# Kernel tuning notes

Measured on AMD Instinct MI355X. Metric: run time of the kernel, lower is better.

## Reference

```python
import jax, jax.numpy as jnp
import numpy as np

DEPTH, DIM, DH, H, DQ, V = 4, 1024, 4096, 8, 128, 32000
B, L = 2, 1024


def setup_inputs() -> dict:
    key = jax.random.key(0)
    ks = iter(jax.random.split(key, 48))
    def nrm(shape, scale=1.0):
        return jax.random.normal(next(ks), shape, jnp.float32) * scale
    d = {}
    d["x"] = nrm((B, L, V))
    d["tin_w"] = nrm((DIM, V), V ** -0.5)
    d["tin_b"] = nrm((DIM,), 0.02)
    d["tout_w"] = nrm((V, DIM), DIM ** -0.5)
    d["tout_b"] = nrm((V,), 0.02)
    d["wq_w"] = nrm((DEPTH, H * DQ, DIM), DIM ** -0.5)
    d["wq_b"] = nrm((DEPTH, H * DQ), 0.02)
    d["wk_w"] = nrm((DEPTH, H * DQ, DIM), DIM ** -0.5)
    d["wk_b"] = nrm((DEPTH, H * DQ), 0.02)
    d["wv_w"] = nrm((DEPTH, H * DQ, DIM), DIM ** -0.5)
    d["wv_b"] = nrm((DEPTH, H * DQ), 0.02)
    d["wo_w"] = nrm((DEPTH, DIM, H * DQ), (H * DQ) ** -0.5)
    d["wo_b"] = nrm((DEPTH, DIM), 0.02)
    d["f1_w"] = nrm((DEPTH, DH, DIM), DIM ** -0.5)
    d["f1_b"] = nrm((DEPTH, DH), 0.02)
    d["f2_w"] = nrm((DEPTH, DIM, DH), DH ** -0.5)
    d["f2_b"] = nrm((DEPTH, DIM), 0.02)
    d["phz_re"] = nrm((DEPTH, H, DQ))
    d["phz_im"] = nrm((DEPTH, H, DQ))
    d["amp"] = nrm((DEPTH, H))
    d["lc_re"] = nrm((DEPTH, H, DQ, DQ), 0.02)
    d["lc_im"] = nrm((DEPTH, H, DQ, DQ), 0.02)
    return d


def _layernorm(x):
    m = x.mean(-1, keepdims=True)
    v = ((x - m) ** 2).mean(-1, keepdims=True)
    return (x - m) * jax.lax.rsqrt(v + 1e-5)


def _retention(x, qw, qb, kw, kb, vw, vb, ow, ob, pre, pim, amp, lcr, lci):
    b, l, _ = x.shape
    q = (x @ qw.T + qb).reshape(b, l, H, DQ)
    k = (x @ kw.T + kb).reshape(b, l, H, DQ)
    v = (x @ vw.T + vb).reshape(b, l, H, DQ)
    pz = pre + 1j * pim                              # [H,DQ] complex
    phase = pz / jnp.abs(pz)                         # unit modulus
    a = jax.nn.sigmoid(amp)                          # [H]
    phazor = phase * a[:, None]
    n = jnp.arange(l)
    pp = phase[None, :, :] ** n[:, None, None]       # [L,H,DQ]
    pp_inv = phase[None, :, :] ** (-n)[:, None, None]
    php = phazor[None, :, :] ** n[:, None, None]
    lc = jax.lax.stop_gradient(lcr + 1j * lci)       # [H,DQ,DQ], detached in torch
    qc = q.astype(jnp.complex64)
    kc = k.astype(jnp.complex64)
    vc = v.astype(jnp.complex64)
    cross = jnp.einsum('blhd,lhd,hde->blhe', qc, php * phazor[None], lc)
    tril = n[:, None] >= n[None, :]
    expn = jnp.where(tril, n[:, None] - n[None, :], 0)           # [L,L]
    mask = jnp.where(tril[None], a[:, None, None] ** expn[None], 0.0)  # [H,L,L]
    qk = jnp.einsum('blhd,bmhd->bhlm', qc * pp[None], kc * pp_inv[None])
    inner = jnp.einsum('bhlm,bmhd->blhd', qk * mask[None].astype(jnp.complex64), vc)
    y = jax.nn.silu((inner + cross).real).reshape(b, l, H * DQ)
    return y @ ow.T + ob


def reference(x, tin_w, tin_b, tout_w, tout_b, wq_w, wq_b, wk_w, wk_b, wv_w, wv_b,
              wo_w, wo_b, f1_w, f1_b, f2_w, f2_b, phz_re, phz_im, amp, lc_re, lc_im):
    h = x @ tin_w.T + tin_b
    for i in range(DEPTH):
        r = _retention(_layernorm(h), wq_w[i], wq_b[i], wk_w[i], wk_b[i],
                       wv_w[i], wv_b[i], wo_w[i], wo_b[i],
                       phz_re[i], phz_im[i], amp[i], lc_re[i], lc_im[i])
        h = h + r
        f = _layernorm(h)
        f = jax.nn.silu(f @ f1_w[i].T + f1_b[i]) @ f2_w[i].T + f2_b[i]
        h = h + f
    return h @ tout_w.T + tout_b
```

## Files before the change

### kernel.cpp

```cpp
#include <hip/hip_runtime.h>
#include <hip/hip_bf16.h>
#include <stdint.h>

#define DEPTH 4
#define DIM   1024
#define DH    4096
#define NH    8
#define DQ    128
#define VOC   32000
#define BATCH 2
#define SEQ   1024
#define ROWS  (BATCH*SEQ)

#define PQKV  ((long long)ROWS*DIM)
#define PQKV3 ((long long)ROWS*3*DIM)
#define PROT  ((long long)BATCH*NH*SEQ*2*DQ)
#define PVT   ((long long)BATCH*NH*DQ*SEQ)
#define PS    ((long long)BATCH*NH*SEQ*SEQ)
#define PMID  ((long long)ROWS*DH)
#define PY    ((long long)ROWS*DIM)

typedef __hip_bfloat16 bf16;
using f32x4  = __attribute__((ext_vector_type(4))) float;
using bf16x8 = __attribute__((ext_vector_type(8))) __bf16;

__device__ __forceinline__ void wpair(bf16* p, long long off, long long plane, float v) {
  bf16 hi = __float2bfloat16(v);
  p[off] = hi;
  p[off + plane] = __float2bfloat16(v - __bfloat162float(hi));
}

__device__ __forceinline__ void gload_lds16(const void* g, void* l) {
  __builtin_amdgcn_global_load_lds(
      (const __attribute__((address_space(1))) void*)g,
      (__attribute__((address_space(3))) void*)(uintptr_t)l,
      16, 0, 0);
}

#define BM 128
#define BN 128
#define BKK 64
#define PL 16384

template<int EPI, int SA, int SB>
__global__ __launch_bounds__(256, (SA || SB) ? 2 : 4)
void gemm_bt(const bf16* __restrict__ A, long long sA, long long pA, int lda,
             const bf16* __restrict__ B, long long sB, long long pB, int ldb, int bmod,
             void* __restrict__ Cv, long long sC, long long pC, int ldc,
             const float* __restrict__ bias, int hmod,
             int M, int N, int K, int ksplit, int causal)
{
  __shared__ int4 sbuf[1024 * (2 + SA + SB)];
  char* Asb = (char*)sbuf;
  char* Bsb = Asb + PL * (1 + SA);

  const int tid  = threadIdx.x;
  const int lane = tid & 63;
  const int wave = tid >> 6;
  const int wr   = wave >> 1;
  const int wc   = wave & 1;
  const int z    = blockIdx.z;
  const int zb   = z / ksplit;
  const int ks   = z - zb * ksplit;
  const int Kc   = K / ksplit;
  const int k0   = ks * Kc;
  const int tm   = blockIdx.x * BM;
  const int tn   = blockIdx.y * BN;

  if (causal == 1 && tn >= tm + BM) return;
  int kend = k0 + Kc;
  if (causal == 2) {
    kend = min(kend, tm + BM);
    if (kend <= k0) return;
  }

  const bf16* Ab = A + (long long)zb * sA;
  const bf16* Bb = B + (long long)(zb % bmod) * sB;

  f32x4 acc[4][4] = {};

  for (int kt = k0; kt < kend; kt += BKK) {
#pragma unroll
    for (int j = 0; j < 4; ++j) {
      int slot0 = j*256 + wave*64;
      int i = slot0 + lane;
      int row = i >> 3;
      int gc  = (i & 7) ^ (row & 7);
      long long ga = (long long)(tm + row) * lda + kt + gc*8;
      long long gb = (long long)(tn + row) * ldb + kt + gc*8;
      gload_lds16(Ab + ga, Asb + slot0*16);
      if (SA) gload_lds16(Ab + pA + ga, Asb + PL + slot0*16);
      gload_lds16(Bb + gb, Bsb + slot0*16);
      if (SB) gload_lds16(Bb + pB + gb, Bsb + PL + slot0*16);
    }
    __syncthreads();
#pragma unroll
    for (int kh = 0; kh < 2; ++kh) {
      const int cb = kh*4 + (lane >> 4);
      int4 avh[4], bvh[4], avl[4], bvl[4];
#pragma unroll
      for (int mi = 0; mi < 4; ++mi) {
        int m = wr*64 + mi*16 + (lane & 15);
        int off = m*128 + ((cb ^ (m & 7)) << 4);
        avh[mi] = *(const int4*)(Asb + off);
        if (SA) avl[mi] = *(const int4*)(Asb + PL + off);
      }
#pragma unroll
      for (int nj = 0; nj < 4; ++nj) {
        int n = wc*64 + nj*16 + (lane & 15);
        int off = n*128 + ((cb ^ (n & 7)) << 4);
        bvh[nj] = *(const int4*)(Bsb + off);
        if (SB) bvl[nj] = *(const int4*)(Bsb + PL + off);
      }
#pragma unroll
      for (int mi = 0; mi < 4; ++mi)
#pragma unroll
        for (int nj = 0; nj < 4; ++nj)
          acc[mi][nj] = __builtin_amdgcn_mfma_f32_16x16x32_bf16(
              __builtin_bit_cast(bf16x8, avh[mi]),
              __builtin_bit_cast(bf16x8, bvh[nj]), acc[mi][nj], 0, 0, 0);
      if (SA)
#pragma unroll
        for (int mi = 0; mi < 4; ++mi)
#pragma unroll
          for (int nj = 0; nj < 4; ++nj)
            acc[mi][nj] = __builtin_amdgcn_mfma_f32_16x16x32_bf16(
                __builtin_bit_cast(bf16x8, avl[mi]),
                __builtin_bit_cast(bf16x8, bvh[nj]), acc[mi][nj], 0, 0, 0);
      if (SB)
#pragma unroll
        for (int mi = 0; mi < 4; ++mi)
#pragma unroll
          for (int nj = 0; nj < 4; ++nj)
            acc[mi][nj] = __builtin_amdgcn_mfma_f32_16x16x32_bf16(
                __builtin_bit_cast(bf16x8, avh[mi]),
                __builtin_bit_cast(bf16x8, bvl[nj]), acc[mi][nj], 0, 0, 0);
    }
    __syncthreads();
  }

  const float* dtab = (EPI == 7) ? bias + (zb % hmod) * (SEQ + 1) : nullptr;
  const int col = lane & 15;
  const int rb  = (lane >> 4) << 2;
  float* Cf = (float*)Cv + (long long)zb * sC;
  bf16*  Ch = (bf16*) Cv + (long long)zb * sC;

#pragma unroll
  for (int mi = 0; mi < 4; ++mi)
#pragma unroll
    for (int nj = 0; nj < 4; ++nj) {
      long long gn = tn + wc*64 + nj*16 + col;
      float bv_ = (EPI != 7 && bias && ks == 0) ? bias[gn] : 0.f;
#pragma unroll
      for (int r = 0; r < 4; ++r) {
        long long gm = tm + wr*64 + mi*16 + rb + r;
        float v = acc[mi][nj][r] + bv_;
        long long off = gm * (long long)ldc + gn;
        if (EPI == 0)      Cf[off] = v;
        else if (EPI == 3) { if (ksplit > 1) atomicAdd(&Cf[off], v); else Cf[off] += v; }
        else if (EPI == 5) wpair(Ch, off, pC, v);
        else if (EPI == 6) wpair(Ch, off, pC, v / (1.f + __expf(-v)));
        else {
          long long dlt = gm - gn;
          float dcy = (dlt >= 0) ? dtab[dlt] : 0.f;
          Ch[off] = __float2bfloat16(acc[mi][nj][r] * dcy);
        }
      }
    }
}

__global__ void castw_kernel(const float* __restrict__ wq, const float* __restrict__ wk,
                             const float* __restrict__ wv, const float* __restrict__ wo,
                             const float* __restrict__ f1, const float* __restrict__ f2,
                             bf16* __restrict__ Wqkv, bf16* __restrict__ Wol,
                             bf16* __restrict__ Wf1, bf16* __restrict__ Wf2) {
  const long long S1 = (long long)DIM*DIM;
  const long long WP = 3*S1;
  long long i = (long long)blockIdx.x * blockDim.x + threadIdx.x;
  if (i < 3*S1) {
    const float* src = (i < S1) ? wq : (i < 2*S1) ? wk : wv;
    float v = src[i & (S1-1)];
    bf16 h = __float2bfloat16(v);
    Wqkv[i] = h;
    Wqkv[i + WP] = __float2bfloat16(v - __bfloat162float(h));
  } else if (i < 4*S1) {
    long long j = i - 3*S1;
    float v = wo[j];
    bf16 h = __float2bfloat16(v);
    Wol[j] = h;
    Wol[j + S1] = __float2bfloat16(v - __bfloat162float(h));
  } else if (i < 8*S1) {
    long long j = i - 4*S1;
    float v = f1[j];
    bf16 h = __float2bfloat16(v);
    Wf1[j] = h;
    Wf1[j + 4*S1] = __float2bfloat16(v - __bfloat162float(h));
  } else if (i < 12*S1) {
    long long j = i - 8*S1;
    Wf2[j] = __float2bfloat16(f2[j]);
  }
}

#define MISC_LC   (NH*DQ*DQ)
#define MISC_B3   (MISC_LC + 3*DIM)
#define MISC_DC   (MISC_B3 + NH*(SEQ+1))
#define MISC_ZR   (MISC_DC + (BATCH*NH*SEQ*DQ)/4)
__global__ void misc_kernel(const float* __restrict__ lcr, const float* __restrict__ lci,
                            bf16* __restrict__ lc,
                            const float* __restrict__ bq, const float* __restrict__ bk,
                            const float* __restrict__ bv, float* __restrict__ qkvbi,
                            const float* __restrict__ amp, float* __restrict__ dtab,
                            float4* __restrict__ retz) {
  long long i = (long long)blockIdx.x * blockDim.x + threadIdx.x;
  if (i < MISC_LC) {
    int d = i & 127, e = (i >> 7) & 127, h = i >> 14;
    float vr = lcr[((long long)h*DQ + d)*DQ + e];
    float vi = lci[((long long)h*DQ + d)*DQ + e];
    long long dst = ((long long)h*DQ + e)*(2*DQ) + d;
    lc[dst]      = __float2bfloat16(vr);
    lc[dst + DQ] = __float2bfloat16(-vi);
  } else if (i < MISC_B3) {
    int j = (int)(i - MISC_LC);
    qkvbi[j] = (j < DIM) ? bq[j] : (j < 2*DIM) ? bk[j - DIM] : bv[j - 2*DIM];
  } else if (i < MISC_DC) {
    int j = (int)(i - MISC_B3);
    int h = j / (SEQ+1), n = j % (SEQ+1);
    float a = 1.f / (1.f + __expf(-amp[h]));
    dtab[j] = powf(a, (float)n);
  } else if (i < MISC_ZR) {
    retz[i - MISC_DC] = float4{0.f, 0.f, 0.f, 0.f};
  }
}

#define TIN_X4 ((long long)ROWS*VOC/4)
#define TIN_W4 (TIN_X4 + (long long)DIM*VOC/4)
#define TIN_H4 (TIN_W4 + (long long)ROWS*DIM/4)
__global__ void tinprep_kernel(const float* __restrict__ x, bf16* __restrict__ xb,
                               const float* __restrict__ tw, bf16* __restrict__ twb,
                               float4* __restrict__ hz) {
  long long i = (long long)blockIdx.x * blockDim.x + threadIdx.x;
  const float* src; bf16* dst; long long j;
  if (i < TIN_X4)      { src = x;  dst = xb;  j = i; }
  else if (i < TIN_W4) { src = tw; dst = twb; j = i - TIN_X4; }
  else if (i < TIN_H4) { hz[i - TIN_W4] = float4{0.f,0.f,0.f,0.f}; return; }
  else return;
  float4 v = ((const float4*)src)[j];
  ushort4 o{__builtin_bit_cast(unsigned short, __float2bfloat16(v.x)),
            __builtin_bit_cast(unsigned short, __float2bfloat16(v.y)),
            __builtin_bit_cast(unsigned short, __float2bfloat16(v.z)),
            __builtin_bit_cast(unsigned short, __float2bfloat16(v.w))};
  ((ushort4*)dst)[j] = o;
}

#define TAIL_H (PQKV)
#define TAIL_W (TAIL_H + (long long)VOC*DIM/4)
__global__ void tailprep_kernel(const float* __restrict__ h, bf16* __restrict__ hb,
                                const float* __restrict__ tw, bf16* __restrict__ twb) {
  long long i = (long long)blockIdx.x * blockDim.x + threadIdx.x;
  if (i < TAIL_H) {
    float v = h[i];
    bf16 hi = __float2bfloat16(v);
    hb[i] = hi;
    hb[i + PQKV] = __float2bfloat16(v - __bfloat162float(hi));
  } else if (i < TAIL_W) {
    long long j = i - TAIL_H;
    float4 v = ((const float4*)tw)[j];
    ushort4 o{__builtin_bit_cast(unsigned short, __float2bfloat16(v.x)),
              __builtin_bit_cast(unsigned short, __float2bfloat16(v.y)),
              __builtin_bit_cast(unsigned short, __float2bfloat16(v.z)),
              __builtin_bit_cast(unsigned short, __float2bfloat16(v.w))};
    ((ushort4*)twb)[j] = o;
  }
}

__global__ void ln_kernel(const float* __restrict__ in, bf16* __restrict__ out) {
  const int row = blockIdx.x;
  const int tid = threadIdx.x;
  const float4 v = ((const float4*)(in + (size_t)row*DIM))[tid];
  float s  = v.x + v.y + v.z + v.w;
  float s2 = v.x*v.x + v.y*v.y + v.z*v.z + v.w*v.w;
#pragma unroll
  for (int o = 32; o > 0; o >>= 1) { s += __shfl_xor(s, o); s2 += __shfl_xor(s2, o); }
  __shared__ float red[8];
  const int wv = tid >> 6;
  if ((tid & 63) == 0) { red[wv] = s; red[4 + wv] = s2; }
  __syncthreads();
  s  = red[0] + red[1] + red[2] + red[3];
  s2 = red[4] + red[5] + red[6] + red[7];
  const float mean = s * (1.f / DIM);
  const float var  = s2 * (1.f / DIM) - mean * mean;
  const float inv  = rsqrtf(var + 1e-5f);
  long long base = (long long)row*DIM + tid*4;
  wpair(out, base + 0, PQKV, (v.x - mean) * inv);
  wpair(out, base + 1, PQKV, (v.y - mean) * inv);
  wpair(out, base + 2, PQKV, (v.z - mean) * inv);
  wpair(out, base + 3, PQKV, (v.w - mean) * inv);
}

__global__ void rotate_kernel(const bf16* __restrict__ qkv,
                              const float* __restrict__ pre, const float* __restrict__ pim,
                              const float* __restrict__ dtab,
                              bf16* __restrict__ qrot, bf16* __restrict__ krot,
                              bf16* __restrict__ qwb) {
  const int d = threadIdx.x, l = blockIdx.x, h = blockIdx.y, b = blockIdx.z;
  const float tr = pre[h*DQ + d], ti = pim[h*DQ + d];
  const float theta = atan2f(ti, tr);
  const long long rowb = (long long)(b*SEQ + l)*(3*DIM) + h*DQ + d;
  const float qv = __bfloat162float(qkv[rowb]) + __bfloat162float(qkv[rowb + PQKV3]);
  const float kv = __bfloat162float(qkv[rowb + DIM]) + __bfloat162float(qkv[rowb + DIM + PQKV3]);
  float sn, cs;
  sincosf(theta * (float)l, &sn, &cs);
  const long long dst = ((long long)(b*NH + h)*SEQ + l)*(2*DQ) + d;
  qrot[dst]      = __float2bfloat16(qv * cs);
  qrot[dst + DQ] = __float2bfloat16(qv * sn);
  krot[dst]      = __float2bfloat16(kv * cs);
  krot[dst + DQ] = __float2bfloat16(kv * sn);
  float sn2, cs2;
  sincosf(theta * (float)(l + 1), &sn2, &cs2);
  const float ad = dtab[h*(SEQ+1) + l + 1];
  qwb[dst]      = __float2bfloat16(qv * ad * cs2);
  qwb[dst + DQ] = __float2bfloat16(qv * ad * sn2);
}

__global__ void vt_kernel(const bf16* __restrict__ qkv, bf16* __restrict__ vt) {
  __shared__ float tile[64][65];
  const int t  = threadIdx.x;
  const int c  = t & 63, r4 = t >> 6;
  const int m0 = blockIdx.x * 64;
  const int d0 = blockIdx.y * 64;
  const int h  = blockIdx.z & (NH - 1);
  const int b  = blockIdx.z >> 3;
#pragma unroll
  for (int rr = 0; rr < 64; rr += 4) {
    const int m = m0 + rr + r4;
    const long long src = (long long)(b*SEQ + m)*(3*DIM) + 2*DIM + h*DQ + d0 + c;
    tile[rr + r4][c] = __bfloat162float(qkv[src]) + __bfloat162float(qkv[src + PQKV3]);
  }
  __syncthreads();
#pragma unroll
  for (int rr = 0; rr < 64; rr += 4) {
    const int d = rr + r4;
    vt[((long long)(b*NH + h)*DQ + d0 + d)*SEQ + m0 + c] = __float2bfloat16(tile[c][d]);
  }
}

__global__ void siluret_kernel(const float* __restrict__ ret, bf16* __restrict__ y) {
  const int d = threadIdx.x, l = blockIdx.x, h = blockIdx.y, b = blockIdx.z;
  float r = ret[((long long)(b*NH + h)*SEQ + l)*DQ + d];
  float s = r / (1.f + __expf(-r));
  wpair(y, ((long long)(b*SEQ + l)*NH + h)*DQ + d, PY, s);
}

extern "C" void kernel_launch(void* const* d_in, const int* in_sizes, int n_in,
                              void* d_out, int out_size, void* d_ws, size_t ws_size,
                              hipStream_t stream) {
  const float* x      = (const float*)d_in[0];
  const float* tin_w  = (const float*)d_in[1];
  const float* tin_b  = (const float*)d_in[2];
  const float* tout_w = (const float*)d_in[3];
  const float* tout_b = (const float*)d_in[4];
  const float* wq_w   = (const float*)d_in[5];
  const float* wq_b   = (const float*)d_in[6];
  const float* wk_w   = (const float*)d_in[7];
  const float* wk_b   = (const float*)d_in[8];
  const float* wv_w   = (const float*)d_in[9];
  const float* wv_b   = (const float*)d_in[10];
  const float* wo_w   = (const float*)d_in[11];
  const float* wo_b   = (const float*)d_in[12];
  const float* f1_w   = (const float*)d_in[13];
  const float* f1_b   = (const float*)d_in[14];
  const float* f2_w   = (const float*)d_in[15];
  const float* f2_b   = (const float*)d_in[16];
  const float* phz_re = (const float*)d_in[17];
  const float* phz_im = (const float*)d_in[18];
  const float* amp    = (const float*)d_in[19];
  const float* lc_re  = (const float*)d_in[20];
  const float* lc_im  = (const float*)d_in[21];
  (void)in_sizes; (void)n_in; (void)out_size; (void)ws_size;

  char* w = (char*)d_ws;
  auto alloc = [&](size_t bytes) {
    char* p = w; w += (bytes + 255) & ~(size_t)255; return p;
  };
  auto palloc = [&](long long elems) {
    return (bf16*)alloc((size_t)elems * 2 * 2);
  };

  const long long WP = 3LL*DIM*DIM;
  float* h     = (float*)alloc((size_t)ROWS*DIM*4);
  float* ret   = (float*)alloc((size_t)BATCH*NH*SEQ*DQ*4);
  float* qkvbi = (float*)alloc((size_t)3*DIM*4);
  float* dtab  = (float*)alloc((size_t)NH*(SEQ+1)*4);
  bf16*  hb    = palloc(PQKV);
  bf16*  Wqkv  = palloc(WP);
  bf16*  Wol   = palloc((long long)DIM*DIM);
  bf16*  Wf1l  = palloc((long long)DH*DIM);
  bf16*  Wf2l  = (bf16*)alloc((size_t)DIM*DH*2);
  bf16*  qkvb  = palloc(PQKV3);
  bf16*  lcc   = (bf16*)alloc((size_t)NH*DQ*2*DQ*2);
  bf16*  Wbig  = (bf16*)alloc((size_t)DIM*VOC*2);
  bf16*  qrot  = (bf16*)alloc((size_t)PROT*2);
  bf16*  krot  = (bf16*)alloc((size_t)PROT*2);
  bf16*  qwb   = (bf16*)alloc((size_t)PROT*2);
  bf16*  vtb   = (bf16*)alloc((size_t)PVT*2);
  bf16*  Sb    = (bf16*)alloc((size_t)PS*2);
  bf16*  mid   = palloc(PMID);
  bf16*  xb = (bf16*)d_out;
  bf16*  yb = qkvb;

  auto gemm = [&](int epi, int sa, int sb, const bf16* A, long long sA, long long pA, int lda,
                  const bf16* B, long long sB, long long pB, int ldb, int bmod,
                  void* C, long long sC, long long pC, int ldc,
                  const float* bias, int hmod, int M, int N, int K, int batch,
                  int ksplit, int causal) {
    dim3 g(M / BM, N / BN, batch * ksplit), blk(256);
    if (epi == 3 && !sa && !sb)      gemm_bt<3,0,0><<<g, blk, 0, stream>>>(A,sA,pA,lda,B,sB,pB,ldb,bmod,C,sC,pC,ldc,bias,hmod,M,N,K,ksplit,causal);
    else if (epi == 7)               gemm_bt<7,0,0><<<g, blk, 0, stream>>>(A,sA,pA,lda,B,sB,pB,ldb,bmod,C,sC,pC,ldc,bias,hmod,M,N,K,ksplit,causal);
    else if (epi == 0 && sa && !sb)  gemm_bt<0,1,0><<<g, blk, 0, stream>>>(A,sA,pA,lda,B,sB,pB,ldb,bmod,C,sC,pC,ldc,bias,hmod,M,N,K,ksplit,causal);
    else if (epi == 3 && sa && !sb)  gemm_bt<3,1,0><<<g, blk, 0, stream>>>(A,sA,pA,lda,B,sB,pB,ldb,bmod,C,sC,pC,ldc,bias,hmod,M,N,K,ksplit,causal);
    else if (epi == 3)               gemm_bt<3,1,1><<<g, blk, 0, stream>>>(A,sA,pA,lda,B,sB,pB,ldb,bmod,C,sC,pC,ldc,bias,hmod,M,N,K,ksplit,causal);
    else if (epi == 5)               gemm_bt<5,1,1><<<g, blk, 0, stream>>>(A,sA,pA,lda,B,sB,pB,ldb,bmod,C,sC,pC,ldc,bias,hmod,M,N,K,ksplit,causal);
    else if (epi == 6)               gemm_bt<6,1,1><<<g, blk, 0, stream>>>(A,sA,pA,lda,B,sB,pB,ldb,bmod,C,sC,pC,ldc,bias,hmod,M,N,K,ksplit,causal);
  };
  const int BIG = 1 << 30;

  {
    long long tot = TIN_H4;
    tinprep_kernel<<<dim3((unsigned)((tot + 255) / 256)), dim3(256), 0, stream>>>(
        x, xb, tin_w, Wbig, (float4*)h);
  }
  gemm(3, 0, 0, xb, 0, 0, VOC, Wbig, 0, 0, VOC, BIG, h, 0, 0, DIM, tin_b, 1,
       ROWS, DIM, VOC, 1, 10, 0);

  for (int i = 0; i < DEPTH; ++i) {
    {
      long long tot = 12LL*DIM*DIM;
      castw_kernel<<<dim3((unsigned)((tot + 255) / 256)), dim3(256), 0, stream>>>(
          wq_w + (size_t)i*DIM*DIM, wk_w + (size_t)i*DIM*DIM, wv_w + (size_t)i*DIM*DIM,
          wo_w + (size_t)i*DIM*DIM, f1_w + (size_t)i*DH*DIM, f2_w + (size_t)i*DIM*DH,
          Wqkv, Wol, Wf1l, Wf2l);
      misc_kernel<<<dim3((unsigned)((MISC_ZR + 255) / 256)), dim3(256), 0, stream>>>(
          lc_re + (size_t)i*NH*DQ*DQ, lc_im + (size_t)i*NH*DQ*DQ, lcc,
          wq_b + i*DIM, wk_b + i*DIM, wv_b + i*DIM, qkvbi,
          amp + i*NH, dtab, (float4*)ret);
    }

    ln_kernel<<<ROWS, 256, 0, stream>>>(h, hb);
    gemm(5, 1, 1, hb, 0, PQKV, DIM, Wqkv, 0, WP, DIM, BIG,
         qkvb, 0, PQKV3, 3*DIM, qkvbi, 1, ROWS, 3*DIM, DIM, 1, 1, 0);
    rotate_kernel<<<dim3(SEQ, NH, BATCH), DQ, 0, stream>>>(
        qkvb, phz_re + i*NH*DQ, phz_im + i*NH*DQ, dtab, qrot, krot, qwb);
    vt_kernel<<<dim3(SEQ/64, DQ/64, BATCH*NH), 256, 0, stream>>>(qkvb, vtb);
    gemm(7, 0, 0, qrot, (long long)SEQ*2*DQ, 0, 2*DQ,
         krot, (long long)SEQ*2*DQ, 0, 2*DQ, BIG,
         Sb, (long long)SEQ*SEQ, 0, SEQ, dtab, NH, SEQ, SEQ, 2*DQ, BATCH*NH, 1, 1);
    gemm(3, 0, 0, Sb, (long long)SEQ*SEQ, 0, SEQ,
         vtb, (long long)DQ*SEQ, 0, SEQ, BIG,
         ret, (long long)SEQ*DQ, 0, DQ, nullptr, 1, SEQ, DQ, SEQ, BATCH*NH, 4, 2);
    gemm(3, 0, 0, qwb, (long long)SEQ*2*DQ, 0, 2*DQ,
         lcc, (long long)DQ*2*DQ, 0, 2*DQ, NH,
         ret, (long long)SEQ*DQ, 0, DQ, nullptr, 1, SEQ, DQ, 2*DQ, BATCH*NH, 2, 0);
    siluret_kernel<<<dim3(SEQ, NH, BATCH), DQ, 0, stream>>>(ret, yb);
    gemm(3, 1, 1, yb, 0, PY, DIM, Wol, 0, (long long)DIM*DIM, DIM, BIG,
         h, 0, 0, DIM, wo_b + i*DIM, 1, ROWS, DIM, DIM, 1, 2, 0);

    ln_kernel<<<ROWS, 256, 0, stream>>>(h, hb);
    gemm(6, 1, 1, hb, 0, PQKV, DIM, Wf1l, 0, (long long)DH*DIM, DIM, BIG,
         mid, 0, PMID, DH, f1_b + i*DH, 1, ROWS, DH, DIM, 1, 1, 0);
    gemm(3, 1, 0, mid, 0, PMID, DH, Wf2l, 0, 0, DH, BIG,
         h, 0, 0, DIM, f2_b + i*DIM, 1, ROWS, DIM, DH, 1, 4, 0);
  }

  tailprep_kernel<<<dim3((unsigned)((TAIL_W + 255) / 256)), dim3(256), 0, stream>>>(
      h, hb, tout_w, Wbig);
  gemm(0, 1, 0, hb, 0, PQKV, DIM, Wbig, 0, 0, DIM, BIG,
       (float*)d_out, 0, 0, VOC, tout_b, 1, ROWS, VOC, DIM, 1, 1, 0);
}
```

Before: 1.864 ms.

## Add 256x256-tile double-buffered MFMA GEMM for token-in, FFN2 and output projections

Adds a new 512-thread GEMM kernel with 256x256 output tiles, XOR-swizzled LDS staged through direct global-to-LDS loads, double buffering, and explicit waitcnt/barrier scheduling with raised priority around MFMA blocks. It replaces the 128x128 gemm_bt for the large-K input projection, the FFN down projection (now split 8 ways with atomics), and the vocabulary output projection. The split-precision A operand (hi/lo planes) is handled by running K as multiple passes over offset planes. The larger tiles are meant to raise arithmetic intensity and cut global traffic, at the cost of more LDS per block and fewer blocks in flight.

```diff
diff --git a/kernel.cpp b/kernel.cpp
--- a/kernel.cpp
+++ b/kernel.cpp
@@ -35,6 +35,134 @@
       (const __attribute__((address_space(1))) void*)g,
       (__attribute__((address_space(3))) void*)(uintptr_t)l,
       16, 0, 0);
+}
+
+#define VMW(n) asm volatile("s_waitcnt vmcnt(" #n ")" ::: "memory")
+
+template<int EPI, int NPASS>
+__global__ __launch_bounds__(512, 2)
+void gemm256(const bf16* __restrict__ A, long long aoff1, long long aoff2, int lda,
+             const bf16* __restrict__ B, long long boff1, long long boff2, int ldb,
+             float* __restrict__ C, int ldc,
+             const float* __restrict__ bias,
+             int M, int N, int K, int ksplit)
+{
+  __shared__ char sh[131072];
+  const int tid  = threadIdx.x;
+  const int lane = tid & 63;
+  const int wid  = tid >> 6;
+  const int wr   = wid >> 2;
+  const int wc   = wid & 3;
+  const int z    = blockIdx.z;
+  const int tm   = blockIdx.x * 256;
+  const int tn   = blockIdx.y * 256;
+  const int nt   = (K * NPASS / 64) / ksplit;
+  const int g0   = z * nt;
+
+  auto stage = [&](int g, int b, int u) {
+    int kt = g * 64;
+    long long ao = 0, bo = 0;
+    if (NPASS >= 2 && kt >= K) {
+      if (NPASS >= 3 && kt >= 2*K) { ao = aoff2; bo = boff2; kt -= 2*K; }
+      else                         { ao = aoff1; bo = boff1; kt -= K; }
+    }
+    int mat, s;
+    switch (u) { case 0: mat=0; s=0; break;  case 1: mat=0; s=2; break;
+                 case 2: mat=1; s=0; break;  case 3: mat=1; s=1; break;
+                 case 4: mat=1; s=2; break;  case 5: mat=1; s=3; break;
+                 case 6: mat=0; s=1; break;  default: mat=0; s=3; break; }
+    int row = s*64 + (tid >> 3);
+    int gc  = (tid & 7) ^ (row & 7);
+    const bf16* src = mat
+        ? (B + bo + (long long)(tn + row) * ldb + kt + gc*8)
+        : (A + ao + (long long)(tm + row) * lda + kt + gc*8);
+    gload_lds16(src, sh + b*65536 + mat*32768 + s*8192 + wid*1024);
+  };
+  auto rdA = [&](int b, int mf, int ks) -> int4 {
+    int m = wr*128 + mf*16 + (lane & 15);
+    int c = ks*4 + (lane >> 4);
+    return *(const int4*)(sh + b*65536 + m*128 + ((c ^ (m & 7)) << 4));
+  };
+  auto rdB = [&](int b, int g, int ks) -> int4 {
+    int n = wc*64 + g*16 + (lane & 15);
+    int c = ks*4 + (lane >> 4);
+    return *(const int4*)(sh + b*65536 + 32768 + n*128 + ((c ^ (n & 7)) << 4));
+  };
+
+  f32x4 acc[8][4] = {};
+  int4  bfr[2][4];
+
+#pragma unroll
+  for (int u = 0; u < 8; ++u) stage(g0, 0, u);
+  VMW(2);
+  __builtin_amdgcn_s_barrier();
+  __builtin_amdgcn_sched_barrier(0);
+
+  for (int j = 0; j < nt; ++j) {
+    const int  b    = j & 1;
+    const bool more = (j + 1 < nt);
+    const int  gn1  = g0 + j + 1;
+#pragma unroll
+    for (int q = 0; q < 4; ++q) {
+      const int mf0 = 2*q, mf1 = 2*q + 1;
+      int4 a00 = rdA(b, mf0, 0), a01 = rdA(b, mf0, 1);
+      int4 a10 = rdA(b, mf1, 0), a11 = rdA(b, mf1, 1);
+      if (q == 0) {
+#pragma unroll
+        for (int ks = 0; ks < 2; ++ks)
+#pragma unroll
+          for (int g = 0; g < 4; ++g) bfr[ks][g] = rdB(b, g, ks);
+      }
+      if (more) { stage(gn1, b^1, 2*q); stage(gn1, b^1, 2*q + 1); }
+      __builtin_amdgcn_s_barrier();
+      asm volatile("s_waitcnt lgkmcnt(0)" ::: "memory");
+      __builtin_amdgcn_sched_barrier(0);
+      __builtin_amdgcn_s_setprio(1);
+#pragma unroll
+      for (int g = 0; g < 4; ++g)
+        acc[mf0][g] = __builtin_amdgcn_mfma_f32_16x16x32_bf16(
+            __builtin_bit_cast(bf16x8, a00), __builtin_bit_cast(bf16x8, bfr[0][g]),
+            acc[mf0][g], 0, 0, 0);
+#pragma unroll
+      for (int g = 0; g < 4; ++g)
+        acc[mf0][g] = __builtin_amdgcn_mfma_f32_16x16x32_bf16(
+            __builtin_bit_cast(bf16x8, a01), __builtin_bit_cast(bf16x8, bfr[1][g]),
+            acc[mf0][g], 0, 0, 0);
+#pragma unroll
+      for (int g = 0; g < 4; ++g)
+        acc[mf1][g] = __builtin_amdgcn_mfma_f32_16x16x32_bf16(
+            __builtin_bit_cast(bf16x8, a10), __builtin_bit_cast(bf16x8, bfr[0][g]),
+            acc[mf1][g], 0, 0, 0);
+#pragma unroll
+      for (int g = 0; g < 4; ++g)
+        acc[mf1][g] = __builtin_amdgcn_mfma_f32_16x16x32_bf16(
+            __builtin_bit_cast(bf16x8, a11), __builtin_bit_cast(bf16x8, bfr[1][g]),
+            acc[mf1][g], 0, 0, 0);
+      __builtin_amdgcn_s_setprio(0);
+      if (q == 1) { if (more) VMW(4); else VMW(0); }
+      if (q == 3) { if (more) VMW(2); }
+      __builtin_amdgcn_s_barrier();
+      __builtin_amdgcn_sched_barrier(0);
+    }
+  }
+
+  const int col = lane & 15;
+  const int rb  = (lane >> 4) << 2;
+#pragma unroll
+  for (int mf = 0; mf < 8; ++mf)
+#pragma unroll
+    for (int g = 0; g < 4; ++g) {
+      long long gn = tn + wc*64 + g*16 + col;
+      float bv = (z == 0 && bias) ? bias[gn] : 0.f;
+#pragma unroll
+      for (int r = 0; r < 4; ++r) {
+        long long gm = tm + wr*128 + mf*16 + rb + r;
+        long long off = gm * (long long)ldc + gn;
+        float v = acc[mf][g][r] + bv;
+        if (EPI == 0) C[off] = v;
+        else { if (ksplit > 1) atomicAdd(&C[off], v); else C[off] += v; }
+      }
+    }
 }
 
 #define BM 128
@@ -416,7 +544,6 @@
     dim3 g(M / BM, N / BN, batch * ksplit), blk(256);
     if (epi == 3 && !sa && !sb)      gemm_bt<3,0,0><<<g, blk, 0, stream>>>(A,sA,pA,lda,B,sB,pB,ldb,bmod,C,sC,pC,ldc,bias,hmod,M,N,K,ksplit,causal);
     else if (epi == 7)               gemm_bt<7,0,0><<<g, blk, 0, stream>>>(A,sA,pA,lda,B,sB,pB,ldb,bmod,C,sC,pC,ldc,bias,hmod,M,N,K,ksplit,causal);
-    else if (epi == 0 && sa && !sb)  gemm_bt<0,1,0><<<g, blk, 0, stream>>>(A,sA,pA,lda,B,sB,pB,ldb,bmod,C,sC,pC,ldc,bias,hmod,M,N,K,ksplit,causal);
     else if (epi == 3 && sa && !sb)  gemm_bt<3,1,0><<<g, blk, 0, stream>>>(A,sA,pA,lda,B,sB,pB,ldb,bmod,C,sC,pC,ldc,bias,hmod,M,N,K,ksplit,causal);
     else if (epi == 3)               gemm_bt<3,1,1><<<g, blk, 0, stream>>>(A,sA,pA,lda,B,sB,pB,ldb,bmod,C,sC,pC,ldc,bias,hmod,M,N,K,ksplit,causal);
     else if (epi == 5)               gemm_bt<5,1,1><<<g, blk, 0, stream>>>(A,sA,pA,lda,B,sB,pB,ldb,bmod,C,sC,pC,ldc,bias,hmod,M,N,K,ksplit,causal);
@@ -424,26 +551,20 @@
   };
   const int BIG = 1 << 30;
 
-  {
-    long long tot = TIN_H4;
-    tinprep_kernel<<<dim3((unsigned)((tot + 255) / 256)), dim3(256), 0, stream>>>(
-        x, xb, tin_w, Wbig, (float4*)h);
-  }
-  gemm(3, 0, 0, xb, 0, 0, VOC, Wbig, 0, 0, VOC, BIG, h, 0, 0, DIM, tin_b, 1,
-       ROWS, DIM, VOC, 1, 10, 0);
+  tinprep_kernel<<<dim3((unsigned)((TIN_H4 + 255) / 256)), dim3(256), 0, stream>>>(
+      x, xb, tin_w, Wbig, (float4*)h);
+  gemm256<3,1><<<dim3(ROWS/256, DIM/256, 10), dim3(512), 0, stream>>>(
+      xb, 0, 0, VOC, Wbig, 0, 0, VOC, h, DIM, tin_b, ROWS, DIM, VOC, 10);
 
   for (int i = 0; i < DEPTH; ++i) {
-    {
-      long long tot = 12LL*DIM*DIM;
-      castw_kernel<<<dim3((unsigned)((tot + 255) / 256)), dim3(256), 0, stream>>>(
-          wq_w + (size_t)i*DIM*DIM, wk_w + (size_t)i*DIM*DIM, wv_w + (size_t)i*DIM*DIM,
-          wo_w + (size_t)i*DIM*DIM, f1_w + (size_t)i*DH*DIM, f2_w + (size_t)i*DIM*DH,
-          Wqkv, Wol, Wf1l, Wf2l);
-      misc_kernel<<<dim3((unsigned)((MISC_ZR + 255) / 256)), dim3(256), 0, stream>>>(
-          lc_re + (size_t)i*NH*DQ*DQ, lc_im + (size_t)i*NH*DQ*DQ, lcc,
-          wq_b + i*DIM, wk_b + i*DIM, wv_b + i*DIM, qkvbi,
-          amp + i*NH, dtab, (float4*)ret);
-    }
+    castw_kernel<<<dim3((unsigned)((12LL*DIM*DIM + 255) / 256)), dim3(256), 0, stream>>>(
+        wq_w + (size_t)i*DIM*DIM, wk_w + (size_t)i*DIM*DIM, wv_w + (size_t)i*DIM*DIM,
+        wo_w + (size_t)i*DIM*DIM, f1_w + (size_t)i*DH*DIM, f2_w + (size_t)i*DIM*DH,
+        Wqkv, Wol, Wf1l, Wf2l);
+    misc_kernel<<<dim3((unsigned)((MISC_ZR + 255) / 256)), dim3(256), 0, stream>>>(
+        lc_re + (size_t)i*NH*DQ*DQ, lc_im + (size_t)i*NH*DQ*DQ, lcc,
+        wq_b + i*DIM, wk_b + i*DIM, wv_b + i*DIM, qkvbi,
+        amp + i*NH, dtab, (float4*)ret);
 
     ln_kernel<<<ROWS, 256, 0, stream>>>(h, hb);
     gemm(5, 1, 1, hb, 0, PQKV, DIM, Wqkv, 0, WP, DIM, BIG,
@@ -467,12 +588,13 @@
     ln_kernel<<<ROWS, 256, 0, stream>>>(h, hb);
     gemm(6, 1, 1, hb, 0, PQKV, DIM, Wf1l, 0, (long long)DH*DIM, DIM, BIG,
          mid, 0, PMID, DH, f1_b + i*DH, 1, ROWS, DH, DIM, 1, 1, 0);
-    gemm(3, 1, 0, mid, 0, PMID, DH, Wf2l, 0, 0, DH, BIG,
-         h, 0, 0, DIM, f2_b + i*DIM, 1, ROWS, DIM, DH, 1, 4, 0);
+    gemm256<3,2><<<dim3(ROWS/256, DIM/256, 8), dim3(512), 0, stream>>>(
+        mid, PMID, 0, DH, Wf2l, 0, 0, DH, h, DIM, f2_b + i*DIM, ROWS, DIM, DH, 8);
   }
 
   tailprep_kernel<<<dim3((unsigned)((TAIL_W + 255) / 256)), dim3(256), 0, stream>>>(
       h, hb, tout_w, Wbig);
-  gemm(0, 1, 0, hb, 0, PQKV, DIM, Wbig, 0, 0, DIM, BIG,
-       (float*)d_out, 0, 0, VOC, tout_b, 1, ROWS, VOC, DIM, 1, 1, 0);
-}
+  gemm256<0,2><<<dim3(ROWS/256, VOC/256, 1), dim3(512), 0, stream>>>(
+      hb, PQKV, 0, DIM, Wbig, 0, 0, DIM, (float*)d_out, VOC, tout_b,
+      ROWS, VOC, DIM, 1);
+}
```

Result: slower. 2.094 ms (+12.3%).
